# Performance work log

Measured on AMD Instinct MI355X. Metric: run time of the kernel, lower is better.

## Reference

```python
import jax, jax.numpy as jnp
import numpy as np

N_NODES = 100000
N_EDGES = 1600000
D_IN, D_HID, N_CLS = 256, 128, 47


def setup_inputs() -> dict:
    key = jax.random.key(0)
    k = jax.random.split(key, 5)
    x = jax.random.normal(k[0], (N_NODES, D_IN), dtype=jnp.float32)
    edge_index = jax.random.randint(k[1], (2, N_EDGES), 0, N_NODES, dtype=jnp.int64)
    W1 = jax.random.normal(k[2], (D_IN, D_HID), dtype=jnp.float32) * 0.05
    b1 = jnp.zeros((D_HID,), dtype=jnp.float32)
    W2 = jax.random.normal(k[3], (D_HID, N_CLS), dtype=jnp.float32) * 0.05
    b2 = jnp.zeros((N_CLS,), dtype=jnp.float32)
    return {"x": x, "edge_index": edge_index, "W1": W1, "b1": b1, "W2": W2, "b2": b2}


def _gcn_conv(x, W, b, src, dst, norm, n):
    # PyG GCNConv: linear transform, normalized scatter-add aggregation, bias after
    h = x @ W                                   # [N, D_out]
    msg = h[src] * norm[:, None]                # gather over edges [E', D_out]
    agg = jax.ops.segment_sum(msg, dst, num_segments=n)
    return agg + b


def reference(x, edge_index, W1, b1, W2, b2):
    n = x.shape[0]
    loop = jnp.arange(n, dtype=edge_index.dtype)
    src = jnp.concatenate([edge_index[0], loop])  # add self-loops
    dst = jnp.concatenate([edge_index[1], loop])
    # symmetric normalization D^-1/2 (A+I) D^-1/2 (degree = in-degree incl. self-loop)
    deg = jax.ops.segment_sum(jnp.ones_like(dst, dtype=x.dtype), dst, num_segments=n)
    dinv = jnp.where(deg > 0, jax.lax.rsqrt(deg), 0.0)
    norm = dinv[src] * dinv[dst]                 # [E']
    h1 = jax.nn.relu(_gcn_conv(x, W1, b1, src, dst, norm, n))
    # dropout with training=False is identity
    out = _gcn_conv(h1, W2, b2, src, dst, norm, n)
    return out
```

## Files before the change

kernel.cpp:

```cpp
#include <hip/hip_runtime.h>
#include <hip/hip_bf16.h>

#define DIN 256
#define DHID 128
#define NCLS 47
#define BSHIFT 9
#define BNODES 512
#define NPART 256
#define BCAPS 9216
#define CHUNKE 6400

typedef __attribute__((ext_vector_type(8))) short short8;
typedef __attribute__((ext_vector_type(4))) float f32x4;

__device__ __forceinline__ short f2bf(float f) {
    __bf16 b = (__bf16)f;
    return __builtin_bit_cast(short, b);
}
__device__ __forceinline__ float bfu(unsigned int u) {
    return __uint_as_float(u << 16);
}
__device__ __forceinline__ float bfh(unsigned int u) {
    return __uint_as_float(u & 0xffff0000u);
}
__device__ __forceinline__ unsigned int pack2(float lo, float hi) {
    return (unsigned int)(unsigned short)f2bf(lo)
         | ((unsigned int)(unsigned short)f2bf(hi) << 16);
}
__device__ __forceinline__ void add8(float* a, uint4 v) {
    a[0] += bfu(v.x); a[1] += bfh(v.x);
    a[2] += bfu(v.y); a[3] += bfh(v.y);
    a[4] += bfu(v.z); a[5] += bfh(v.z);
    a[6] += bfu(v.w); a[7] += bfh(v.w);
}
__device__ __forceinline__ void fma8(float* a, uint4 v, float d) {
    a[0] += d * bfu(v.x); a[1] += d * bfh(v.x);
    a[2] += d * bfu(v.y); a[3] += d * bfh(v.y);
    a[4] += d * bfu(v.z); a[5] += d * bfh(v.z);
    a[6] += d * bfu(v.w); a[7] += d * bfh(v.w);
}

__global__ __launch_bounds__(256) void k_prep_hist(const float* __restrict__ W1,
                                                   const float* __restrict__ W2,
                                                   short* __restrict__ W1s,
                                                   short* __restrict__ W2s,
                                                   const int* __restrict__ dst,
                                                   int* __restrict__ ghist,
                                                   int E, int NB, int chunk) {
    __shared__ int lh[256];
    int blk = blockIdx.x, t = threadIdx.x;
    if (blk < 16) {
        int tid = blk * 256 + t;
        int frag = tid >> 6, lane = tid & 63;
        int kt = frag >> 3, nt = frag & 7;
        int quad = lane >> 4, col = lane & 15;
        #pragma unroll
        for (int j = 0; j < 8; ++j) {
            int k = kt * 32 + quad * 8 + j;
            W1s[(size_t)tid * 8 + j] = f2bf(W1[k * DHID + nt * 16 + col]);
        }
    } else if (blk < 20) {
        int tid = (blk - 16) * 256 + t;
        int frag = tid >> 6, lane = tid & 63;
        int kt = frag >> 2, nt = frag & 3;
        int quad = lane >> 4, col = lane & 15;
        int c = nt * 16 + col;
        #pragma unroll
        for (int j = 0; j < 8; ++j) {
            int k = kt * 32 + quad * 8 + j;
            float v = (c < NCLS) ? W2[k * NCLS + c] : 0.0f;
            W2s[(size_t)tid * 8 + j] = f2bf(v);
        }
    } else {
        int p = blk - 20;
        for (int i = t; i < NB; i += 256) lh[i] = 0;
        __syncthreads();
        int lo = p * chunk, hi = min(E, lo + chunk);
        for (int i = lo + t; i < hi; i += 256)
            atomicAdd(&lh[dst[i] >> BSHIFT], 1);
        __syncthreads();
        for (int i = t; i < NB; i += 256) ghist[(size_t)i * NPART + p] = lh[i];
    }
}

__global__ __launch_bounds__(256) void k_scatter_gemm1(const int* __restrict__ src,
                                                       const int* __restrict__ dst,
                                                       const int* __restrict__ ghist,
                                                       int* __restrict__ btot,
                                                       unsigned int* __restrict__ bbuf,
                                                       int E, int NB, int chunk,
                                                       const float* __restrict__ x,
                                                       const short* __restrict__ W1s,
                                                       short* __restrict__ hb, int n) {
    __shared__ __align__(16) char smem[65536];
    int blk = blockIdx.x, t = threadIdx.x;

    if (blk < NPART) {
        unsigned int* stage = (unsigned int*)smem;
        int* sdest = (int*)(smem + 25600);
        int* lcur  = (int*)(smem + 51200);
        int* gdst  = (int*)(smem + 52224);
        int* wsum  = (int*)(smem + 53248);

        int tot = 0, pref = 0, mine = 0;
        if (t < NB) {
            const int* gp = ghist + (size_t)t * NPART;
            mine = gp[blk];
            #pragma unroll 8
            for (int p = 0; p < NPART; ++p) {
                int v = gp[p];
                tot += v;
                pref += (p < blk) ? v : 0;
            }
        }
        if (blk == 0 && t < NB) btot[t] = tot;

        int lane = t & 63, w = t >> 6;
        int incl = tot;
        #pragma unroll
        for (int off = 1; off < 64; off <<= 1) {
            int u = __shfl_up(incl, off, 64);
            if (lane >= off) incl += u;
        }
        if (lane == 63) wsum[w] = incl;
        __syncthreads();
        int wadd = 0;
        for (int i = 0; i < w; ++i) wadd += wsum[i];
        int bbase = wadd + incl - tot;
        __syncthreads();
        incl = mine;
        #pragma unroll
        for (int off = 1; off < 64; off <<= 1) {
            int u = __shfl_up(incl, off, 64);
            if (lane >= off) incl += u;
        }
        if (lane == 63) wsum[w] = incl;
        __syncthreads();
        wadd = 0;
        for (int i = 0; i < w; ++i) wadd += wsum[i];
        int ex = wadd + incl - mine;

        lcur[t] = ex;
        gdst[t] = bbase + pref - ex;
        __syncthreads();

        int lo = blk * chunk, hi = min(E, lo + chunk), cnt = hi - lo;
        for (int i = lo + t; i < hi; i += 256) {
            int d = dst[i];
            int b = d >> BSHIFT;
            int slot = atomicAdd(&lcur[b], 1);
            stage[slot] = (unsigned int)src[i] | ((unsigned int)(d & (BNODES - 1)) << 17);
            sdest[slot] = gdst[b] + slot;
        }
        __syncthreads();
        for (int i = t; i < cnt; i += 256)
            bbuf[sdest[i]] = stage[i];
    } else {
        short* lw = (short*)smem;
        {
            const uint4* g = (const uint4*)W1s;
            uint4* l = (uint4*)lw;
            for (int i = t; i < 4096; i += 256) l[i] = g[i];
        }
        __syncthreads();

        int bid = blk - NPART;
        int wave = t >> 6, lane = t & 63;
        int quad = lane >> 4, lrow = lane & 15;
        long long rowbase = (long long)bid * 128 + wave * 32;

        f32x4 acc[2][8];
        #pragma unroll
        for (int rt = 0; rt < 2; ++rt)
            #pragma unroll
            for (int nt = 0; nt < 8; ++nt) acc[rt][nt] = (f32x4){0.f, 0.f, 0.f, 0.f};

        const short8* lf = (const short8*)lw;

        #pragma unroll
        for (int kt = 0; kt < 8; ++kt) {
            int k0 = kt * 32 + quad * 8;
            short8 a[2];
            #pragma unroll
            for (int rt = 0; rt < 2; ++rt) {
                long long row = rowbase + rt * 16 + lrow;
                float4 v0 = {0.f,0.f,0.f,0.f}, v1 = {0.f,0.f,0.f,0.f};
                if (row < n) {
                    const float* xp = x + row * DIN + k0;
                    v0 = *(const float4*)xp;
                    v1 = *(const float4*)(xp + 4);
                }
                short8 av;
                av[0] = f2bf(v0.x); av[1] = f2bf(v0.y); av[2] = f2bf(v0.z); av[3] = f2bf(v0.w);
                av[4] = f2bf(v1.x); av[5] = f2bf(v1.y); av[6] = f2bf(v1.z); av[7] = f2bf(v1.w);
                a[rt] = av;
            }
            #pragma unroll
            for (int nt = 0; nt < 8; ++nt) {
                short8 b = lf[(kt * 8 + nt) * 64 + lane];
                acc[0][nt] = __builtin_amdgcn_mfma_f32_16x16x32_bf16(a[0], b, acc[0][nt], 0, 0, 0);
                acc[1][nt] = __builtin_amdgcn_mfma_f32_16x16x32_bf16(a[1], b, acc[1][nt], 0, 0, 0);
            }
        }
        #pragma unroll
        for (int rt = 0; rt < 2; ++rt)
            #pragma unroll
            for (int nt = 0; nt < 8; ++nt)
                #pragma unroll
                for (int r = 0; r < 4; ++r) {
                    long long row = rowbase + rt * 16 + quad * 4 + r;
                    if (row < n) hb[row * DHID + nt * 16 + lrow] = f2bf(acc[rt][nt][r]);
                }
    }
}

__device__ __forceinline__ void scan_btot(const int* __restrict__ btot, int NB,
                                          int* lbase, int* wsum) {
    int t = threadIdx.x;
    int v = (t < NB) ? btot[t] : 0;
    int incl = v;
    int lane = t & 63, w = t >> 6;
    #pragma unroll
    for (int off = 1; off < 64; off <<= 1) {
        int u = __shfl_up(incl, off, 64);
        if (lane >= off) incl += u;
    }
    if (lane == 63) wsum[w] = incl;
    __syncthreads();
    int wadd = 0;
    for (int i = 0; i < w; ++i) wadd += wsum[i];
    lbase[t] = wadd + incl - v;
    __syncthreads();
}

__global__ __launch_bounds__(256) void k_bsort(const int* __restrict__ btot,
                                               unsigned int* __restrict__ bbuf,
                                               int* __restrict__ degi,
                                               int* __restrict__ beg,
                                               float* __restrict__ dinv, int n, int NB) {
    __shared__ unsigned int stage[BCAPS];
    __shared__ int hist[BNODES];
    __shared__ int cur[BNODES];
    __shared__ int lbase[256];
    __shared__ int wsum[4];

    int b = blockIdx.x, t = threadIdx.x;
    scan_btot(btot, NB, lbase, wsum);
    int cnt = min(btot[b], BCAPS);
    int gbase = lbase[b];
    int node0 = b << BSHIFT;

    if (t < 128) { ((int2*)hist)[t] = (int2){0, 0}; ((int2*)hist)[t + 128] = (int2){0, 0}; }
    __syncthreads();

    for (int i = t; i < cnt; i += 256) {
        unsigned int p = bbuf[gbase + i];
        stage[i] = p;
        atomicAdd(&hist[p >> 17], 1);
    }
    __syncthreads();

    int v0 = hist[2 * t], v1 = hist[2 * t + 1];
    int s = v0 + v1;
    int incl = s;
    int lane = t & 63, w = t >> 6;
    #pragma unroll
    for (int off = 1; off < 64; off <<= 1) {
        int u = __shfl_up(incl, off, 64);
        if (lane >= off) incl += u;
    }
    if (lane == 63) wsum[w] = incl;
    __syncthreads();
    int wadd = 0;
    for (int i = 0; i < w; ++i) wadd += wsum[i];
    int ex = wadd + incl - s;
    cur[2 * t] = ex;
    cur[2 * t + 1] = ex + v0;
    int nodeA = node0 + 2 * t, nodeB = node0 + 2 * t + 1;
    if (nodeA < n) {
        degi[nodeA] = v0;
        beg[nodeA]  = gbase + ex;
        dinv[nodeA] = rsqrtf((float)(v0 + 1));
    }
    if (nodeB < n) {
        degi[nodeB] = v1;
        beg[nodeB]  = gbase + ex + v0;
        dinv[nodeB] = rsqrtf((float)(v1 + 1));
    }
    __syncthreads();

    for (int i = t; i < cnt; i += 256) {
        unsigned int p = stage[i];
        int slot = atomicAdd(&cur[p >> 17], 1);
        bbuf[gbase + slot] = p & 0x1FFFFu;
    }
}

__global__ __launch_bounds__(1024) void k_g1g2(const int* __restrict__ beg,
                          const int* __restrict__ degi,
                          const int* __restrict__ ssrc, const float* __restrict__ dinv,
                          const uint4* __restrict__ hb4, const float* __restrict__ b1,
                          const short* __restrict__ W2s,
                          short* __restrict__ h2b, int n) {
    __shared__ short lw[8192];
    __shared__ short h1s[16 * 136];
    ((uint4*)lw)[threadIdx.x & 1023] = ((const uint4*)W2s)[threadIdx.x & 1023];

    int wv = threadIdx.x >> 6;
    int t  = threadIdx.x & 63;
    int grp = t >> 4, sub = t & 15;
    int node = blockIdx.x * 16 + wv;
    bool alive = node < n;
    int cnt = alive ? degi[node] : 0;
    int bg  = alive ? beg[node]  : 0;

    float a[8] = {0.f,0.f,0.f,0.f,0.f,0.f,0.f,0.f};
    int k = 0;
    for (; k + 16 <= cnt; k += 16) {
        int s[4];
        #pragma unroll
        for (int q = 0; q < 4; ++q) s[q] = ssrc[bg + k + grp * 4 + q];
        float dv[4]; uint4 v[4];
        #pragma unroll
        for (int q = 0; q < 4; ++q) { dv[q] = dinv[s[q]]; v[q] = hb4[(size_t)s[q] * 16 + sub]; }
        #pragma unroll
        for (int q = 0; q < 4; ++q) fma8(a, v[q], dv[q]);
    }
    for (; k < cnt; k += 4) {
        int idx = k + grp;
        if (idx < cnt) {
            int s = ssrc[bg + idx];
            fma8(a, hb4[(size_t)s * 16 + sub], dinv[s]);
        }
    }
    #pragma unroll
    for (int j = 0; j < 8; ++j) {
        a[j] += __shfl_xor(a[j], 16);
        a[j] += __shfl_xor(a[j], 32);
    }

    if (grp == 0) {
        uint4 o = {0u, 0u, 0u, 0u};
        if (alive) {
            uint4 sv = hb4[(size_t)node * 16 + sub];
            float di = dinv[node], dd = di * di;
            float4 bA = ((const float4*)b1)[sub * 2];
            float4 bB = ((const float4*)b1)[sub * 2 + 1];
            float v0 = fmaxf(di * a[0] + dd * bfu(sv.x) + bA.x, 0.f);
            float v1 = fmaxf(di * a[1] + dd * bfh(sv.x) + bA.y, 0.f);
            float v2 = fmaxf(di * a[2] + dd * bfu(sv.y) + bA.z, 0.f);
            float v3 = fmaxf(di * a[3] + dd * bfh(sv.y) + bA.w, 0.f);
            float v4 = fmaxf(di * a[4] + dd * bfu(sv.z) + bB.x, 0.f);
            float v5 = fmaxf(di * a[5] + dd * bfh(sv.z) + bB.y, 0.f);
            float v6 = fmaxf(di * a[6] + dd * bfu(sv.w) + bB.z, 0.f);
            float v7 = fmaxf(di * a[7] + dd * bfh(sv.w) + bB.w, 0.f);
            o.x = pack2(v0, v1);
            o.y = pack2(v2, v3);
            o.z = pack2(v4, v5);
            o.w = pack2(v6, v7);
        }
        *(uint4*)(h1s + wv * 136 + sub * 8) = o;
    }
    __syncthreads();

    if (wv < 4) {
        int quad = t >> 4, lrow = t & 15;
        f32x4 acc = (f32x4){0.f, 0.f, 0.f, 0.f};
        const short8* lf = (const short8*)lw;
        #pragma unroll
        for (int kt = 0; kt < 4; ++kt) {
            short8 aa = *(const short8*)(h1s + lrow * 136 + kt * 32 + quad * 8);
            acc = __builtin_amdgcn_mfma_f32_16x16x32_bf16(aa, lf[(kt * 4 + wv) * 64 + t], acc, 0, 0, 0);
        }
        #pragma unroll
        for (int r = 0; r < 4; ++r) {
            int nodeo = blockIdx.x * 16 + quad * 4 + r;
            if (nodeo < n) h2b[(size_t)nodeo * 64 + wv * 16 + lrow] = f2bf(acc[r] * dinv[nodeo]);
        }
    }
}

__global__ __launch_bounds__(256) void k_gather2(const int* __restrict__ beg,
                          const int* __restrict__ degi,
                          const int* __restrict__ ssrc, const float* __restrict__ dinv,
                          const uint4* __restrict__ h2b4, const float* __restrict__ b2,
                          float* __restrict__ out, int n) {
    int node = blockIdx.x * 4 + (threadIdx.x >> 6);
    int t = threadIdx.x & 63;
    if (node >= n) return;
    int cnt = degi[node];
    int bg  = beg[node];
    int grp = t >> 3, sub = t & 7;

    float a[8] = {0.f,0.f,0.f,0.f,0.f,0.f,0.f,0.f};
    int k = 0;
    for (; k + 16 <= cnt; k += 16) {
        int s0 = ssrc[bg + k + grp], s1 = ssrc[bg + k + 8 + grp];
        uint4 v0 = h2b4[(size_t)s0 * 8 + sub];
        uint4 v1 = h2b4[(size_t)s1 * 8 + sub];
        add8(a, v0); add8(a, v1);
    }
    for (; k < cnt; k += 8) {
        int idx = k + grp;
        if (idx < cnt) {
            int s = ssrc[bg + idx];
            add8(a, h2b4[(size_t)s * 8 + sub]);
        }
    }
    if (grp == 0) add8(a, h2b4[(size_t)node * 8 + sub]);

    #pragma unroll
    for (int j = 0; j < 8; ++j) {
        a[j] += __shfl_xor(a[j], 8);
        a[j] += __shfl_xor(a[j], 16);
        a[j] += __shfl_xor(a[j], 32);
    }

    if (grp == 0) {
        float di = dinv[node];
        #pragma unroll
        for (int j = 0; j < 8; ++j) {
            int c = sub * 8 + j;
            if (c < NCLS) out[(size_t)node * NCLS + c] = di * a[j] + b2[c];
        }
    }
}

extern "C" void kernel_launch(void* const* d_in, const int* in_sizes, int n_in,
                              void* d_out, int out_size, void* d_ws, size_t ws_size,
                              hipStream_t stream) {
    const float* x  = (const float*)d_in[0];
    const int*   ei = (const int*)d_in[1];
    const float* W1 = (const float*)d_in[2];
    const float* b1 = (const float*)d_in[3];
    const float* W2 = (const float*)d_in[4];
    const float* b2 = (const float*)d_in[5];

    const int n = in_sizes[0] / DIN;
    const int E = in_sizes[1] / 2;
    const int* src = ei;
    const int* dst = ei + E;
    float* out = (float*)d_out;

    const int NB = (n + BNODES - 1) >> BSHIFT;
    const int chunk = (E + NPART - 1) / NPART;

    char* w = (char*)d_ws;
    int*   ghist = (int*)w;                    w += (size_t)NB * NPART * 4;
    int*   btot  = (int*)w;                    w += ((size_t)NB * 4 + 15) & ~15ull;
    int*   degi  = (int*)w;                    w += (size_t)n * 4;
    int*   beg   = (int*)w;                    w += (size_t)n * 4;
    float* dinv  = (float*)w;                  w += (size_t)n * 4;
    short* W1s   = (short*)w;                  w += (size_t)32768 * 2;
    short* W2s   = (short*)w;                  w += (size_t)8192 * 2;
    unsigned int* bbuf = (unsigned int*)w;     w += (size_t)E * 4;
    short* hb    = (short*)w;                  w += (size_t)n * DHID * 2;
    short* h2b   = (short*)w;                  w += (size_t)n * 64 * 2;

    k_prep_hist<<<20 + NPART, 256, 0, stream>>>(W1, W2, W1s, W2s, dst, ghist, E, NB, chunk);
    k_scatter_gemm1<<<NPART + (n + 127) / 128, 256, 0, stream>>>(src, dst, ghist, btot, bbuf,
                                                                 E, NB, chunk, x, W1s, hb, n);
    k_bsort<<<NB, 256, 0, stream>>>(btot, bbuf, degi, beg, dinv, n, NB);
    k_g1g2<<<(n + 15) / 16, 1024, 0, stream>>>(beg, degi, (const int*)bbuf, dinv,
                                               (const uint4*)hb, b1, W2s, h2b, n);
    k_gather2<<<(n + 3) / 4, 256, 0, stream>>>(beg, degi, (const int*)bbuf, dinv,
                                               (const uint4*)h2b, b2, out, n);
}
```

Baseline: 409.6 us.

## Split fused gather1+GEMM2 kernel into separate gather and MFMA GEMM kernels

Replaces the fused 1024-thread kernel, which aggregated layer-1 messages and immediately ran the layer-2 MFMA per 16-node tile, with two kernels. The first is a 256-thread gather that writes the ReLU'd h1 to a new bf16 buffer. The second is a standalone MFMA GEMM that processes 64 rows per block with W2 staged in LDS. This removes the per-block W2 LDS load, the block-wide barrier and the idle waves during the MFMA phase, and allows better occupancy for the gather. In exchange it adds an extra global write and read of h1 and one more kernel launch.

```diff
diff --git a/kernel.cpp b/kernel.cpp
--- a/kernel.cpp
+++ b/kernel.cpp
@@ -296,23 +296,17 @@
     }
 }
 
-__global__ __launch_bounds__(1024) void k_g1g2(const int* __restrict__ beg,
+__global__ __launch_bounds__(256) void k_gather1(const int* __restrict__ beg,
                           const int* __restrict__ degi,
                           const int* __restrict__ ssrc, const float* __restrict__ dinv,
                           const uint4* __restrict__ hb4, const float* __restrict__ b1,
-                          const short* __restrict__ W2s,
-                          short* __restrict__ h2b, int n) {
-    __shared__ short lw[8192];
-    __shared__ short h1s[16 * 136];
-    ((uint4*)lw)[threadIdx.x & 1023] = ((const uint4*)W2s)[threadIdx.x & 1023];
-
-    int wv = threadIdx.x >> 6;
-    int t  = threadIdx.x & 63;
+                          uint4* __restrict__ h1u4, int n) {
+    int node = blockIdx.x * 4 + (threadIdx.x >> 6);
+    int t = threadIdx.x & 63;
+    if (node >= n) return;
+    int cnt = degi[node];
+    int bg  = beg[node];
     int grp = t >> 4, sub = t & 15;
-    int node = blockIdx.x * 16 + wv;
-    bool alive = node < n;
-    int cnt = alive ? degi[node] : 0;
-    int bg  = alive ? beg[node]  : 0;
 
     float a[8] = {0.f,0.f,0.f,0.f,0.f,0.f,0.f,0.f};
     int k = 0;
@@ -333,6 +327,7 @@
             fma8(a, hb4[(size_t)s * 16 + sub], dinv[s]);
         }
     }
+
     #pragma unroll
     for (int j = 0; j < 8; ++j) {
         a[j] += __shfl_xor(a[j], 16);
@@ -340,44 +335,71 @@
     }
 
     if (grp == 0) {
-        uint4 o = {0u, 0u, 0u, 0u};
-        if (alive) {
-            uint4 sv = hb4[(size_t)node * 16 + sub];
-            float di = dinv[node], dd = di * di;
-            float4 bA = ((const float4*)b1)[sub * 2];
-            float4 bB = ((const float4*)b1)[sub * 2 + 1];
-            float v0 = fmaxf(di * a[0] + dd * bfu(sv.x) + bA.x, 0.f);
-            float v1 = fmaxf(di * a[1] + dd * bfh(sv.x) + bA.y, 0.f);
-            float v2 = fmaxf(di * a[2] + dd * bfu(sv.y) + bA.z, 0.f);
-            float v3 = fmaxf(di * a[3] + dd * bfh(sv.y) + bA.w, 0.f);
-            float v4 = fmaxf(di * a[4] + dd * bfu(sv.z) + bB.x, 0.f);
-            float v5 = fmaxf(di * a[5] + dd * bfh(sv.z) + bB.y, 0.f);
-            float v6 = fmaxf(di * a[6] + dd * bfu(sv.w) + bB.z, 0.f);
-            float v7 = fmaxf(di * a[7] + dd * bfh(sv.w) + bB.w, 0.f);
-            o.x = pack2(v0, v1);
-            o.y = pack2(v2, v3);
-            o.z = pack2(v4, v5);
-            o.w = pack2(v6, v7);
-        }
-        *(uint4*)(h1s + wv * 136 + sub * 8) = o;
-    }
-    __syncthreads();
-
-    if (wv < 4) {
-        int quad = t >> 4, lrow = t & 15;
-        f32x4 acc = (f32x4){0.f, 0.f, 0.f, 0.f};
-        const short8* lf = (const short8*)lw;
-        #pragma unroll
-        for (int kt = 0; kt < 4; ++kt) {
-            short8 aa = *(const short8*)(h1s + lrow * 136 + kt * 32 + quad * 8);
-            acc = __builtin_amdgcn_mfma_f32_16x16x32_bf16(aa, lf[(kt * 4 + wv) * 64 + t], acc, 0, 0, 0);
-        }
+        uint4 sv = hb4[(size_t)node * 16 + sub];
+        float di = dinv[node], dd = di * di;
+        float4 bA = ((const float4*)b1)[sub * 2];
+        float4 bB = ((const float4*)b1)[sub * 2 + 1];
+        float v0 = fmaxf(di * a[0] + dd * bfu(sv.x) + bA.x, 0.f);
+        float v1 = fmaxf(di * a[1] + dd * bfh(sv.x) + bA.y, 0.f);
+        float v2 = fmaxf(di * a[2] + dd * bfu(sv.y) + bA.z, 0.f);
+        float v3 = fmaxf(di * a[3] + dd * bfh(sv.y) + bA.w, 0.f);
+        float v4 = fmaxf(di * a[4] + dd * bfu(sv.z) + bB.x, 0.f);
+        float v5 = fmaxf(di * a[5] + dd * bfh(sv.z) + bB.y, 0.f);
+        float v6 = fmaxf(di * a[6] + dd * bfu(sv.w) + bB.z, 0.f);
+        float v7 = fmaxf(di * a[7] + dd * bfh(sv.w) + bB.w, 0.f);
+        uint4 o;
+        o.x = pack2(v0, v1);
+        o.y = pack2(v2, v3);
+        o.z = pack2(v4, v5);
+        o.w = pack2(v6, v7);
+        h1u4[(size_t)node * 16 + sub] = o;
+    }
+}
+
+__global__ __launch_bounds__(256) void k_gemm2_mfma(const short* __restrict__ h1b,
+                                                    const short* __restrict__ W2s,
+                                                    const float* __restrict__ dinv,
+                                                    short* __restrict__ h2b, int n) {
+    __shared__ short lw[8192];
+    {
+        const uint4* g = (const uint4*)W2s;
+        uint4* l = (uint4*)lw;
+        for (int i = threadIdx.x; i < 1024; i += 256) l[i] = g[i];
+    }
+    __syncthreads();
+
+    int wave = threadIdx.x >> 6, lane = threadIdx.x & 63;
+    int quad = lane >> 4, lrow = lane & 15;
+    long long row0 = (long long)blockIdx.x * 64 + wave * 16;
+
+    f32x4 acc[4];
+    #pragma unroll
+    for (int nt = 0; nt < 4; ++nt) acc[nt] = (f32x4){0.f, 0.f, 0.f, 0.f};
+
+    const short8* lf = (const short8*)lw;
+
+    #pragma unroll
+    for (int kt = 0; kt < 4; ++kt) {
+        long long row = row0 + lrow;
+        short8 a = (short8){0,0,0,0,0,0,0,0};
+        if (row < n) a = *(const short8*)(h1b + row * DHID + kt * 32 + quad * 8);
+        #pragma unroll
+        for (int nt = 0; nt < 4; ++nt)
+            acc[nt] = __builtin_amdgcn_mfma_f32_16x16x32_bf16(a, lf[(kt * 4 + nt) * 64 + lane], acc[nt], 0, 0, 0);
+    }
+    float dvv[4];
+    #pragma unroll
+    for (int r = 0; r < 4; ++r) {
+        long long row = row0 + quad * 4 + r;
+        dvv[r] = (row < n) ? dinv[row] : 0.f;
+    }
+    #pragma unroll
+    for (int nt = 0; nt < 4; ++nt)
         #pragma unroll
         for (int r = 0; r < 4; ++r) {
-            int nodeo = blockIdx.x * 16 + quad * 4 + r;
-            if (nodeo < n) h2b[(size_t)nodeo * 64 + wv * 16 + lrow] = f2bf(acc[r] * dinv[nodeo]);
-        }
-    }
+            long long row = row0 + quad * 4 + r;
+            if (row < n) h2b[row * 64 + nt * 16 + lrow] = f2bf(acc[nt][r] * dvv[r]);
+        }
 }
 
 __global__ __launch_bounds__(256) void k_gather2(const int* __restrict__ beg,
@@ -455,14 +477,17 @@
     short* W2s   = (short*)w;                  w += (size_t)8192 * 2;
     unsigned int* bbuf = (unsigned int*)w;     w += (size_t)E * 4;
     short* hb    = (short*)w;                  w += (size_t)n * DHID * 2;
+    short* h1b   = (short*)w;                  w += (size_t)n * DHID * 2;
     short* h2b   = (short*)w;                  w += (size_t)n * 64 * 2;
 
     k_prep_hist<<<20 + NPART, 256, 0, stream>>>(W1, W2, W1s, W2s, dst, ghist, E, NB, chunk);
     k_scatter_gemm1<<<NPART + (n + 127) / 128, 256, 0, stream>>>(src, dst, ghist, btot, bbuf,
                                                                  E, NB, chunk, x, W1s, hb, n);
     k_bsort<<<NB, 256, 0, stream>>>(btot, bbuf, degi, beg, dinv, n, NB);
-    k_g1g2<<<(n + 15) / 16, 1024, 0, stream>>>(beg, degi, (const int*)bbuf, dinv,
-                                               (const uint4*)hb, b1, W2s, h2b, n);
+    k_gather1<<<(n + 3) / 4, 256, 0, stream>>>(beg, degi, (const int*)bbuf, dinv,
+                                               (const uint4*)hb, b1,
+                                               (uint4*)h1b, n);
+    k_gemm2_mfma<<<(n + 63) / 64, 256, 0, stream>>>(h1b, W2s, dinv, h2b, n);
     k_gather2<<<(n + 3) / 4, 256, 0, stream>>>(beg, degi, (const int*)bbuf, dinv,
                                                (const uint4*)h2b, b2, out, n);
 }
```

After: 402.6 us. No clear change (-1.7%).
